# Kernel optimization log

Measured on AMD Instinct MI355X. Metric: run time of the kernel, lower is better.

Reference implementation:

```python
import jax, jax.numpy as jnp
import numpy as np

DIM = 192
RES = 64
NUM_HEADS = 4
H_SP, W_SP = RES, 4  # idx == 0
SCALE = (DIM // NUM_HEADS) ** (-0.5)


def conv2d(x, w, b, pad, groups=1):
    y = jax.lax.conv_general_dilated(
        x, w, window_strides=(1, 1), padding=[(pad, pad), (pad, pad)],
        dimension_numbers=("NCHW", "OIHW", "NCHW"), feature_group_count=groups)
    return y + b[None, :, None, None]


def img2windows(img, H_sp, W_sp):
    B, C, H, W = img.shape
    x = img.reshape(B, C, H // H_sp, H_sp, W // W_sp, W_sp)
    return jnp.transpose(x, (0, 2, 4, 3, 5, 1)).reshape(-1, H_sp * W_sp, C)


def windows2img(w, H_sp, W_sp, H, W):
    Bw = w.shape[0]
    B = Bw // ((H // H_sp) * (W // W_sp))
    x = w.reshape(B, H // H_sp, W // W_sp, H_sp, W_sp, -1)
    return jnp.transpose(x, (0, 5, 1, 3, 2, 4)).reshape(B, -1, H, W)


def im2cswin(x):
    w = img2windows(x, H_SP, W_SP)  # [B', L, C]
    Bw, L, C = w.shape
    return jnp.transpose(w.reshape(Bw, L, NUM_HEADS, C // NUM_HEADS), (0, 2, 1, 3))


def setup_inputs() -> dict:
    key = jax.random.key(0)
    ks = jax.random.split(key, 11)
    s = 0.02
    return {
        "x": jax.random.normal(ks[0], (32, DIM, RES, RES), jnp.float32),
        "w_qk": jax.random.normal(ks[1], (2 * DIM, DIM, 1, 1), jnp.float32) * s,
        "b_qk": jnp.zeros((2 * DIM,), jnp.float32),
        "w_q5": jax.random.normal(ks[2], (DIM, 1, 5, 5), jnp.float32) * s,
        "b_q5": jnp.zeros((DIM,), jnp.float32),
        "w_k5": jax.random.normal(ks[3], (DIM, 1, 5, 5), jnp.float32) * s,
        "b_k5": jnp.zeros((DIM,), jnp.float32),
        "w_v": jax.random.normal(ks[4], (DIM, DIM, 1, 1), jnp.float32) * s,
        "b_v": jnp.zeros((DIM,), jnp.float32),
        "w_cape": jax.random.normal(ks[5], (DIM, 1, 5, 5), jnp.float32) * s,
        "b_cape": jnp.zeros((DIM,), jnp.float32),
    }


def reference(x, w_qk, b_qk, w_q5, b_q5, w_k5, b_k5, w_v, b_v, w_cape, b_cape):
    B, C, H, W = x.shape
    qk = conv2d(x, w_qk, b_qk, pad=0)
    q, k = jnp.split(qk, 2, axis=1)
    v = conv2d(x, w_v, b_v, pad=0)
    cape = conv2d(v, w_cape, b_cape, pad=2, groups=DIM)  # depthwise 5x5
    q = im2cswin(conv2d(q, w_q5, b_q5, pad=2, groups=DIM) + cape)
    k = im2cswin(conv2d(k, w_k5, b_k5, pad=2, groups=DIM) + cape)
    vw = im2cswin(v)
    q = q * SCALE
    attn = jnp.einsum("whqd,whkd->whqk", q, k)  # windows, heads, L, L
    attn = jax.nn.softmax(attn, axis=-1)
    out = jnp.einsum("whqk,whkd->whqd", attn, vw)
    Bw = out.shape[0]
    out = jnp.transpose(out, (0, 2, 1, 3)).reshape(Bw, H_SP * W_SP, C)
    return windows2img(out, H_SP, W_SP, H, W) + cape
```

## Files before the change

### kernel.cpp

```cpp
#include <hip/hip_runtime.h>

typedef short short8 __attribute__((ext_vector_type(8)));
typedef float f32x4 __attribute__((ext_vector_type(4)));

#define BATCH 32
#define DIM 192
#define RES 64
#define HW 4096
#define NH 4
#define DH 48
#define NWIN 16
#define LTOK 256
#define BUFE (BATCH * DIM * HW)
#define SCALE_Q 0.14433756729740643f

__device__ __forceinline__ unsigned short f2bf(float f) {
  unsigned int u = __builtin_bit_cast(unsigned int, f);
  u += 0x7fffu + ((u >> 16) & 1u);
  return (unsigned short)(u >> 16);
}
__device__ __forceinline__ float bf2f(unsigned short h) {
  unsigned int u = ((unsigned int)h) << 16;
  return __builtin_bit_cast(float, u);
}
__device__ __forceinline__ f32x4 mfma16(short8 a, short8 b, f32x4 c) {
  return __builtin_amdgcn_mfma_f32_16x16x32_bf16(a, b, c, 0, 0, 0);
}

__global__ __launch_bounds__(256, 2) void k1_conv1x1(
    const float* __restrict__ x, const float* __restrict__ w_qk,
    const float* __restrict__ b_qk, const float* __restrict__ w_v,
    const float* __restrict__ b_v, unsigned short* __restrict__ q_raw,
    unsigned short* __restrict__ k_raw, unsigned short* __restrict__ v_buf) {
  __shared__ unsigned short Al[96 * 200];
  __shared__ unsigned short Bl[64 * 200];
  const int tid = threadIdx.x;
  const int octile = blockIdx.x;
  const int pixtile = blockIdx.y;
  const int b = blockIdx.z;
  const int oc0 = octile * 96;
  const int pix0 = pixtile * 64;

  {
    const float* wsrc = (oc0 < 384) ? (w_qk + oc0 * DIM) : (w_v + (oc0 - 384) * DIM);
    for (int it = 0; it < 18; ++it) {
      int u = it * 256 + tid;
      int oc = u / 48, ic4 = u % 48;
      float4 f = *(const float4*)(wsrc + oc * DIM + ic4 * 4);
      uint2 pk;
      pk.x = (unsigned int)f2bf(f.x) | ((unsigned int)f2bf(f.y) << 16);
      pk.y = (unsigned int)f2bf(f.z) | ((unsigned int)f2bf(f.w) << 16);
      *(uint2*)&Al[oc * 200 + ic4 * 4] = pk;
    }
  }
  {
    const float* xb = x + (size_t)b * (DIM * HW) + pix0;
    int px = tid & 63;
    int icq = tid >> 6;
    for (int it = 0; it < 6; ++it) {
      int ic8 = icq + it * 4;
      const float* p = xb + (size_t)(ic8 * 8) * HW + px;
      unsigned short h[8];
#pragma unroll
      for (int j = 0; j < 8; ++j) h[j] = f2bf(p[(size_t)j * HW]);
      uint4 pk;
      pk.x = h[0] | ((unsigned int)h[1] << 16);
      pk.y = h[2] | ((unsigned int)h[3] << 16);
      pk.z = h[4] | ((unsigned int)h[5] << 16);
      pk.w = h[6] | ((unsigned int)h[7] << 16);
      *(uint4*)&Bl[px * 200 + ic8 * 8] = pk;
    }
  }
  __syncthreads();

  const int lane = tid & 63, wv = tid >> 6;
  const int quad = lane >> 4, col = lane & 15;
  const int m0 = (wv >> 1) * 48, n0 = (wv & 1) * 32;

  f32x4 acc[3][2];
#pragma unroll
  for (int fm = 0; fm < 3; ++fm)
#pragma unroll
    for (int fn = 0; fn < 2; ++fn) {
      acc[fm][fn][0] = 0.f; acc[fm][fn][1] = 0.f;
      acc[fm][fn][2] = 0.f; acc[fm][fn][3] = 0.f;
    }

#pragma unroll
  for (int ks = 0; ks < 6; ++ks) {
    short8 a[3], bb[2];
#pragma unroll
    for (int fm = 0; fm < 3; ++fm)
      a[fm] = *(const short8*)&Al[(m0 + fm * 16 + col) * 200 + ks * 32 + quad * 8];
#pragma unroll
    for (int fn = 0; fn < 2; ++fn)
      bb[fn] = *(const short8*)&Bl[(n0 + fn * 16 + col) * 200 + ks * 32 + quad * 8];
#pragma unroll
    for (int fm = 0; fm < 3; ++fm)
#pragma unroll
      for (int fn = 0; fn < 2; ++fn) acc[fm][fn] = mfma16(a[fm], bb[fn], acc[fm][fn]);
  }

  unsigned short* dst;
  int ocbase;
  if (oc0 < 192) { dst = q_raw; ocbase = oc0; }
  else if (oc0 < 384) { dst = k_raw; ocbase = oc0 - 192; }
  else { dst = v_buf; ocbase = oc0 - 384; }
#pragma unroll
  for (int fm = 0; fm < 3; ++fm) {
#pragma unroll
    for (int r = 0; r < 4; ++r) {
      int ocoff = m0 + fm * 16 + quad * 4 + r;
      int ocg = oc0 + ocoff;
      float bias = (ocg < 384) ? b_qk[ocg] : b_v[ocg - 384];
      size_t rowoff = ((size_t)b * DIM + (ocbase + ocoff)) * HW;
#pragma unroll
      for (int fn = 0; fn < 2; ++fn) {
        int pix = pix0 + n0 + fn * 16 + col;
        dst[rowoff + pix] = f2bf(acc[fm][fn][r] + bias);
      }
    }
  }
}

__global__ __launch_bounds__(256) void k2_cape(
    const unsigned short* __restrict__ v_buf, const float* __restrict__ w_cape,
    const float* __restrict__ b_cape, float* __restrict__ cape_out) {
  const int c = blockIdx.y, b = blockIdx.z;
  const int h = blockIdx.x * 16 + (threadIdx.x >> 4);
  const int w4 = threadIdx.x & 15;
  const unsigned short* vp = v_buf + ((size_t)b * DIM + c) * HW;
  float wk[25];
#pragma unroll
  for (int i = 0; i < 25; ++i) wk[i] = w_cape[c * 25 + i];
  float acc[4];
  float bz = b_cape[c];
  acc[0] = acc[1] = acc[2] = acc[3] = bz;
#pragma unroll
  for (int dy = 0; dy < 5; ++dy) {
    int hr = h + dy - 2;
    float row[8];
    if (hr >= 0 && hr < RES) {
      const unsigned short* rp = vp + hr * RES + w4 * 4 - 2;
#pragma unroll
      for (int j = 0; j < 4; ++j) {
        int wc = w4 * 4 - 2 + 2 * j;
        unsigned int d = (wc >= 0 && wc < RES) ? *(const unsigned int*)(rp + 2 * j) : 0u;
        row[2 * j] = bf2f((unsigned short)(d & 0xffff));
        row[2 * j + 1] = bf2f((unsigned short)(d >> 16));
      }
    } else {
#pragma unroll
      for (int j = 0; j < 8; ++j) row[j] = 0.f;
    }
#pragma unroll
    for (int wj = 0; wj < 4; ++wj)
#pragma unroll
      for (int dx = 0; dx < 5; ++dx) acc[wj] += row[wj + dx] * wk[dy * 5 + dx];
  }
  float4 o;
  o.x = acc[0]; o.y = acc[1]; o.z = acc[2]; o.w = acc[3];
  *(float4*)&cape_out[((size_t)b * DIM + c) * HW + h * RES + w4 * 4] = o;
}

__global__ __launch_bounds__(256) void k3_dw(
    const unsigned short* __restrict__ src, const float* __restrict__ w5,
    const float* __restrict__ b5, const float* __restrict__ cape,
    unsigned short* __restrict__ dst_w, float scale) {
  __shared__ unsigned short patch[64 * 168];
  __shared__ unsigned short outS[64 * 72];
  const int lid = blockIdx.x;
  const int xx = lid & 7;
  const int ii = lid >> 3;
  const int b = xx * 4 + ii / 192;
  const int rem = ii % 192;
  const int wb = rem / 12;
  const int rr2 = rem % 12;
  const int ct = rr2 >> 2, ht = rr2 & 3;
  const int c0 = ct * 64, h0 = ht * 16;
  const int tid = threadIdx.x;

  for (int it = 0; it < 5; ++it) {
    int u = it * 256 + tid;
    int c = u / 20, rr = u % 20;
    int hr = h0 - 2 + rr;
    uint4 pk;
    pk.x = pk.y = pk.z = pk.w = 0u;
    if (hr >= 0 && hr < RES) {
      const unsigned short* rp =
          src + ((size_t)b * DIM + c0 + c) * HW + hr * RES + wb * 4 - 2;
      unsigned int dw[4];
#pragma unroll
      for (int j = 0; j < 4; ++j) {
        int wc = wb * 4 - 2 + 2 * j;
        dw[j] = (wc >= 0 && wc < RES) ? *(const unsigned int*)(rp + 2 * j) : 0u;
      }
      pk.x = dw[0]; pk.y = dw[1]; pk.z = dw[2]; pk.w = dw[3];
    }
    *(uint4*)&patch[c * 168 + rr * 8] = pk;
  }
  __syncthreads();

  const int c = tid >> 2, hq = tid & 3;
  float wk[25];
#pragma unroll
  for (int i = 0; i < 25; ++i) wk[i] = w5[(c0 + c) * 25 + i];
  float bz = b5[c0 + c];
  float acc[4][4];
#pragma unroll
  for (int j = 0; j < 4; ++j)
#pragma unroll
    for (int wm = 0; wm < 4; ++wm) acc[j][wm] = bz;

#pragma unroll
  for (int rel = 0; rel < 8; ++rel) {
    int p = hq * 4 + rel;
    uint4 pk = *(const uint4*)&patch[c * 168 + p * 8];
    float f8[8];
    f8[0] = bf2f((unsigned short)(pk.x & 0xffff));
    f8[1] = bf2f((unsigned short)(pk.x >> 16));
    f8[2] = bf2f((unsigned short)(pk.y & 0xffff));
    f8[3] = bf2f((unsigned short)(pk.y >> 16));
    f8[4] = bf2f((unsigned short)(pk.z & 0xffff));
    f8[5] = bf2f((unsigned short)(pk.z >> 16));
    f8[6] = bf2f((unsigned short)(pk.w & 0xffff));
    f8[7] = bf2f((unsigned short)(pk.w >> 16));
#pragma unroll
    for (int j = 0; j < 4; ++j) {
      int dy = rel - j;
      if (dy >= 0 && dy <= 4) {
#pragma unroll
        for (int wm = 0; wm < 4; ++wm)
#pragma unroll
          for (int dx = 0; dx < 5; ++dx) acc[j][wm] += f8[wm + dx] * wk[dy * 5 + dx];
      }
    }
  }

  size_t cpbase = ((size_t)b * DIM + c0 + c) * HW + (size_t)wb * 4;
#pragma unroll
  for (int j = 0; j < 4; ++j) {
    int h = h0 + hq * 4 + j;
    float4 cp = *(const float4*)&cape[cpbase + (size_t)h * RES];
    int lb = (hq * 4 + j) * 4;
    outS[(lb + 0) * 72 + c] = f2bf((acc[j][0] + cp.x) * scale);
    outS[(lb + 1) * 72 + c] = f2bf((acc[j][1] + cp.y) * scale);
    outS[(lb + 2) * 72 + c] = f2bf((acc[j][2] + cp.z) * scale);
    outS[(lb + 3) * 72 + c] = f2bf((acc[j][3] + cp.w) * scale);
  }
  __syncthreads();

  const size_t obase = ((size_t)(b * NWIN + wb) * LTOK + (size_t)h0 * 4) * DIM + c0;
  for (int it = 0; it < 2; ++it) {
    int u = it * 256 + tid;
    int ll = u >> 3, part = u & 7;
    *(uint4*)&dst_w[obase + (size_t)ll * DIM + part * 8] =
        *(const uint4*)&outS[ll * 72 + part * 8];
  }
}

#define KSTR 56
#define VSTR 256
#define PSTR 264

__global__ __launch_bounds__(256, 2) void k5_attn(
    const unsigned short* __restrict__ qf_w, const unsigned short* __restrict__ kf_w,
    const unsigned short* __restrict__ v_buf, unsigned short* __restrict__ out_w) {
  __shared__ unsigned short smem[29184];
  unsigned short* Kl = smem;
  unsigned short* Pl = smem;
  unsigned short* Vl = smem + 16896;

  const int lid = blockIdx.x;
  const int xx = lid & 7;
  const int ii = lid >> 3;
  const int b = (xx << 2) | (ii >> 8);
  const int rem = ii & 255;
  const int wb = rem >> 4;
  const int hd = (rem >> 2) & 3;
  const int qt = rem & 3;
  const int wi = b * NWIN + wb;

  const int tid = threadIdx.x, lane = tid & 63, wv = tid >> 6;
  const int quad = lane >> 4, col = lane & 15;
  const int q = qt * 64 + wv * 16 + col;

  const unsigned short* qp = qf_w + ((size_t)wi * LTOK + q) * DIM + hd * DH;
  short8 z8 = {0, 0, 0, 0, 0, 0, 0, 0};
  short8 bq0 = *(const short8*)(qp + quad * 8);
  short8 bq1 = z8;
  if (quad < 2) bq1 = *(const short8*)(qp + 32 + quad * 8);

  {
    const unsigned short* ks = kf_w + (size_t)wi * LTOK * DIM + hd * DH;
    for (int it = 0; it < 6; ++it) {
      int u = it * 256 + tid;
      int kl = u / 6, part = u % 6;
      *(uint4*)&Kl[kl * KSTR + part * 8] = *(const uint4*)(ks + (size_t)kl * DIM + part * 8);
    }
  }
  {
    const unsigned short* vs = v_buf + ((size_t)b * DIM + hd * DH) * HW + wb * 4;
    for (int it = 0; it < 12; ++it) {
      int u = it * 256 + tid;
      int d = u >> 6, h = u & 63;
      int kl8 = h >> 1;
      int off = ((kl8 ^ (d & 7)) * 8) + (h & 1) * 4;
      *(uint2*)&Vl[d * VSTR + off] = *(const uint2*)(vs + (size_t)d * HW + h * RES);
    }
  }
  __syncthreads();

  f32x4 s[16];
#pragma unroll
  for (int i = 0; i < 16; ++i) { s[i][0] = 0.f; s[i][1] = 0.f; s[i][2] = 0.f; s[i][3] = 0.f; }
#pragma unroll
  for (int fm = 0; fm < 16; ++fm) {
    short8 a0 = *(const short8*)&Kl[(fm * 16 + col) * KSTR + quad * 8];
    s[fm] = mfma16(a0, bq0, s[fm]);
  }
#pragma unroll
  for (int fm = 0; fm < 16; ++fm) {
    short8 a1 = z8;
    if (quad < 2) a1 = *(const short8*)&Kl[(fm * 16 + col) * KSTR + 32 + quad * 8];
    s[fm] = mfma16(a1, bq1, s[fm]);
  }

  float mx = s[0][0];
#pragma unroll
  for (int fm = 0; fm < 16; ++fm)
#pragma unroll
    for (int r = 0; r < 4; ++r) mx = fmaxf(mx, s[fm][r]);
  mx = fmaxf(mx, __shfl_xor(mx, 16));
  mx = fmaxf(mx, __shfl_xor(mx, 32));
  float sm = 0.f;
#pragma unroll
  for (int fm = 0; fm < 16; ++fm)
#pragma unroll
    for (int r = 0; r < 4; ++r) {
      float e = __expf(s[fm][r] - mx);
      s[fm][r] = e;
      sm += e;
    }
  sm += __shfl_xor(sm, 16);
  sm += __shfl_xor(sm, 32);
  float inv = 1.f / sm;

  __syncthreads();

  {
    unsigned short* Pw = Pl + (wv * 16 + col) * PSTR;
#pragma unroll
    for (int fm = 0; fm < 16; ++fm) {
      uint2 pk;
      pk.x = (unsigned int)f2bf(s[fm][0] * inv) | ((unsigned int)f2bf(s[fm][1] * inv) << 16);
      pk.y = (unsigned int)f2bf(s[fm][2] * inv) | ((unsigned int)f2bf(s[fm][3] * inv) << 16);
      *(uint2*)&Pw[fm * 16 + quad * 4] = pk;
    }
  }

  f32x4 o[3];
#pragma unroll
  for (int i = 0; i < 3; ++i) { o[i][0] = 0.f; o[i][1] = 0.f; o[i][2] = 0.f; o[i][3] = 0.f; }
#pragma unroll
  for (int ksi = 0; ksi < 8; ++ksi) {
    short8 a = *(const short8*)&Pl[(wv * 16 + col) * PSTR + ksi * 32 + quad * 8];
#pragma unroll
    for (int fn = 0; fn < 3; ++fn) {
      int d = fn * 16 + col;
      short8 bb = *(const short8*)&Vl[d * VSTR + (((ksi * 4 + quad) ^ (d & 7)) * 8)];
      o[fn] = mfma16(a, bb, o[fn]);
    }
  }

  {
    unsigned short* dst = out_w + ((size_t)wi * LTOK + qt * 64 + wv * 16) * DIM + hd * DH;
#pragma unroll
    for (int fn = 0; fn < 3; ++fn)
#pragma unroll
      for (int r = 0; r < 4; ++r)
        dst[(size_t)(quad * 4 + r) * DIM + fn * 16 + col] = f2bf(o[fn][r]);
  }
}

__global__ __launch_bounds__(256) void k6_final(
    const unsigned short* __restrict__ out_w, float* __restrict__ io) {
  __shared__ float tile[16 * 528];
  const int ht = blockIdx.x, ct = blockIdx.y, b = blockIdx.z;
  const int c0 = ct * 16, h0 = ht * 8;
  const int tid = threadIdx.x;
  for (int it = 0; it < 4; ++it) {
    int u = it * 256 + tid;
    int chunk = u & 1, l5 = (u >> 1) & 31, wb = u >> 6;
    const unsigned short* p =
        out_w + ((size_t)(b * NWIN + wb) * LTOK + (size_t)(h0 * 4 + l5)) * DIM + c0 + chunk * 8;
    uint4 pk = *(const uint4*)p;
    int h = l5 >> 2, wm = l5 & 3;
    float* t = &tile[(chunk * 8) * 528 + h * 66 + wb * 4 + wm];
    t[0 * 528] = bf2f((unsigned short)(pk.x & 0xffff));
    t[1 * 528] = bf2f((unsigned short)(pk.x >> 16));
    t[2 * 528] = bf2f((unsigned short)(pk.y & 0xffff));
    t[3 * 528] = bf2f((unsigned short)(pk.y >> 16));
    t[4 * 528] = bf2f((unsigned short)(pk.z & 0xffff));
    t[5 * 528] = bf2f((unsigned short)(pk.z >> 16));
    t[6 * 528] = bf2f((unsigned short)(pk.w & 0xffff));
    t[7 * 528] = bf2f((unsigned short)(pk.w >> 16));
  }
  __syncthreads();
  for (int it = 0; it < 8; ++it) {
    int u = it * 256 + tid;
    int w16 = u & 15, h = (u >> 4) & 7, c = u >> 7;
    size_t g = ((size_t)b * DIM + c0 + c) * HW + (size_t)(h0 + h) * RES + w16 * 4;
    float4 cp = *(const float4*)&io[g];
    float4 ov;
    ov.x = tile[c * 528 + h * 66 + w16 * 4 + 0] + cp.x;
    ov.y = tile[c * 528 + h * 66 + w16 * 4 + 1] + cp.y;
    ov.z = tile[c * 528 + h * 66 + w16 * 4 + 2] + cp.z;
    ov.w = tile[c * 528 + h * 66 + w16 * 4 + 3] + cp.w;
    *(float4*)&io[g] = ov;
  }
}

extern "C" void kernel_launch(void* const* d_in, const int* in_sizes, int n_in,
                              void* d_out, int out_size, void* d_ws, size_t ws_size,
                              hipStream_t stream) {
  (void)in_sizes; (void)n_in; (void)out_size; (void)ws_size;
  const float* x = (const float*)d_in[0];
  const float* w_qk = (const float*)d_in[1];
  const float* b_qk = (const float*)d_in[2];
  const float* w_q5 = (const float*)d_in[3];
  const float* b_q5 = (const float*)d_in[4];
  const float* w_k5 = (const float*)d_in[5];
  const float* b_k5 = (const float*)d_in[6];
  const float* w_v = (const float*)d_in[7];
  const float* b_v = (const float*)d_in[8];
  const float* w_cape = (const float*)d_in[9];
  const float* b_cape = (const float*)d_in[10];
  float* out = (float*)d_out;

  unsigned short* ws = (unsigned short*)d_ws;
  unsigned short* buf0 = ws;
  unsigned short* buf1 = ws + (size_t)BUFE;
  unsigned short* buf2 = ws + (size_t)BUFE * 2;
  unsigned short* buf3 = ws + (size_t)BUFE * 3;

  k1_conv1x1<<<dim3(6, 64, 32), 256, 0, stream>>>(x, w_qk, b_qk, w_v, b_v, buf0, buf1, buf2);
  k2_cape<<<dim3(4, 192, 32), 256, 0, stream>>>(buf2, w_cape, b_cape, out);
  k3_dw<<<dim3(6144), 256, 0, stream>>>(buf0, w_q5, b_q5, out, buf3, SCALE_Q);
  k3_dw<<<dim3(6144), 256, 0, stream>>>(buf1, w_k5, b_k5, out, buf0, 1.0f);
  k5_attn<<<dim3(8192), 256, 0, stream>>>(buf3, buf0, buf2, buf1);
  k6_final<<<dim3(8, 12, 32), 256, 0, stream>>>(buf1, out);
}
```

Before: 780.6 us.

## Pre-convert 1x1 conv weights to bf16 and loop all output-channel tiles per block

Adds a small kernel that converts the qk and v 1x1 weights to bf16 once, written into a scratch buffer. The 1x1 conv kernel now handles all six 96-channel output tiles inside each block. The x tile is converted and staged in shared memory once, so it is no longer re-read and re-converted six times. The next weight tile is prefetched into registers while the current tile is computed, at the cost of higher register use, fewer blocks (2048) and an extra launch.

```diff
diff --git a/kernel.cpp b/kernel.cpp
--- a/kernel.cpp
+++ b/kernel.cpp
@@ -27,32 +27,31 @@
   return __builtin_amdgcn_mfma_f32_16x16x32_bf16(a, b, c, 0, 0, 0);
 }
 
+__global__ __launch_bounds__(256) void k0_wcvt(
+    const float* __restrict__ w_qk, const float* __restrict__ w_v,
+    unsigned short* __restrict__ wbf) {
+  int u = blockIdx.x * 256 + threadIdx.x;
+  int i4 = u * 4;
+  const float* src = (i4 < 2 * DIM * DIM) ? (w_qk + i4) : (w_v + (i4 - 2 * DIM * DIM));
+  float4 f = *(const float4*)src;
+  uint2 pk;
+  pk.x = (unsigned int)f2bf(f.x) | ((unsigned int)f2bf(f.y) << 16);
+  pk.y = (unsigned int)f2bf(f.z) | ((unsigned int)f2bf(f.w) << 16);
+  *(uint2*)&wbf[i4] = pk;
+}
+
 __global__ __launch_bounds__(256, 2) void k1_conv1x1(
-    const float* __restrict__ x, const float* __restrict__ w_qk,
-    const float* __restrict__ b_qk, const float* __restrict__ w_v,
-    const float* __restrict__ b_v, unsigned short* __restrict__ q_raw,
-    unsigned short* __restrict__ k_raw, unsigned short* __restrict__ v_buf) {
+    const float* __restrict__ x, const unsigned short* __restrict__ wbf,
+    const float* __restrict__ b_qk, const float* __restrict__ b_v,
+    unsigned short* __restrict__ q_raw, unsigned short* __restrict__ k_raw,
+    unsigned short* __restrict__ v_buf) {
   __shared__ unsigned short Al[96 * 200];
   __shared__ unsigned short Bl[64 * 200];
   const int tid = threadIdx.x;
-  const int octile = blockIdx.x;
-  const int pixtile = blockIdx.y;
-  const int b = blockIdx.z;
-  const int oc0 = octile * 96;
+  const int pixtile = blockIdx.x;
+  const int b = blockIdx.y;
   const int pix0 = pixtile * 64;
 
-  {
-    const float* wsrc = (oc0 < 384) ? (w_qk + oc0 * DIM) : (w_v + (oc0 - 384) * DIM);
-    for (int it = 0; it < 18; ++it) {
-      int u = it * 256 + tid;
-      int oc = u / 48, ic4 = u % 48;
-      float4 f = *(const float4*)(wsrc + oc * DIM + ic4 * 4);
-      uint2 pk;
-      pk.x = (unsigned int)f2bf(f.x) | ((unsigned int)f2bf(f.y) << 16);
-      pk.y = (unsigned int)f2bf(f.z) | ((unsigned int)f2bf(f.w) << 16);
-      *(uint2*)&Al[oc * 200 + ic4 * 4] = pk;
-    }
-  }
   {
     const float* xb = x + (size_t)b * (DIM * HW) + pix0;
     int px = tid & 63;
@@ -71,55 +70,84 @@
       *(uint4*)&Bl[px * 200 + ic8 * 8] = pk;
     }
   }
-  __syncthreads();
 
   const int lane = tid & 63, wv = tid >> 6;
   const int quad = lane >> 4, col = lane & 15;
   const int m0 = (wv >> 1) * 48, n0 = (wv & 1) * 32;
 
-  f32x4 acc[3][2];
-#pragma unroll
-  for (int fm = 0; fm < 3; ++fm)
-#pragma unroll
-    for (int fn = 0; fn < 2; ++fn) {
-      acc[fm][fn][0] = 0.f; acc[fm][fn][1] = 0.f;
-      acc[fm][fn][2] = 0.f; acc[fm][fn][3] = 0.f;
-    }
-
-#pragma unroll
-  for (int ks = 0; ks < 6; ++ks) {
-    short8 a[3], bb[2];
+  uint4 wreg[9];
+#pragma unroll
+  for (int it = 0; it < 9; ++it) {
+    int u = it * 256 + tid;
+    int row = u / 24, part = u % 24;
+    wreg[it] = *(const uint4*)(wbf + row * 192 + part * 8);
+  }
+
+  for (int t = 0; t < 6; ++t) {
+#pragma unroll
+    for (int it = 0; it < 9; ++it) {
+      int u = it * 256 + tid;
+      int row = u / 24, part = u % 24;
+      *(uint4*)&Al[row * 200 + part * 8] = wreg[it];
+    }
+    __syncthreads();
+
+    if (t < 5) {
+      const unsigned short* wsrc = wbf + (t + 1) * (96 * 192);
+#pragma unroll
+      for (int it = 0; it < 9; ++it) {
+        int u = it * 256 + tid;
+        int row = u / 24, part = u % 24;
+        wreg[it] = *(const uint4*)(wsrc + row * 192 + part * 8);
+      }
+    }
+
+    f32x4 acc[3][2];
 #pragma unroll
     for (int fm = 0; fm < 3; ++fm)
-      a[fm] = *(const short8*)&Al[(m0 + fm * 16 + col) * 200 + ks * 32 + quad * 8];
-#pragma unroll
-    for (int fn = 0; fn < 2; ++fn)
-      bb[fn] = *(const short8*)&Bl[(n0 + fn * 16 + col) * 200 + ks * 32 + quad * 8];
-#pragma unroll
-    for (int fm = 0; fm < 3; ++fm)
-#pragma unroll
-      for (int fn = 0; fn < 2; ++fn) acc[fm][fn] = mfma16(a[fm], bb[fn], acc[fm][fn]);
-  }
-
-  unsigned short* dst;
-  int ocbase;
-  if (oc0 < 192) { dst = q_raw; ocbase = oc0; }
-  else if (oc0 < 384) { dst = k_raw; ocbase = oc0 - 192; }
-  else { dst = v_buf; ocbase = oc0 - 384; }
-#pragma unroll
-  for (int fm = 0; fm < 3; ++fm) {
-#pragma unroll
-    for (int r = 0; r < 4; ++r) {
-      int ocoff = m0 + fm * 16 + quad * 4 + r;
-      int ocg = oc0 + ocoff;
-      float bias = (ocg < 384) ? b_qk[ocg] : b_v[ocg - 384];
-      size_t rowoff = ((size_t)b * DIM + (ocbase + ocoff)) * HW;
 #pragma unroll
       for (int fn = 0; fn < 2; ++fn) {
-        int pix = pix0 + n0 + fn * 16 + col;
-        dst[rowoff + pix] = f2bf(acc[fm][fn][r] + bias);
-      }
-    }
+        acc[fm][fn][0] = 0.f; acc[fm][fn][1] = 0.f;
+        acc[fm][fn][2] = 0.f; acc[fm][fn][3] = 0.f;
+      }
+
+#pragma unroll
+    for (int ks = 0; ks < 6; ++ks) {
+      short8 a[3], bb[2];
+#pragma unroll
+      for (int fm = 0; fm < 3; ++fm)
+        a[fm] = *(const short8*)&Al[(m0 + fm * 16 + col) * 200 + ks * 32 + quad * 8];
+#pragma unroll
+      for (int fn = 0; fn < 2; ++fn)
+        bb[fn] = *(const short8*)&Bl[(n0 + fn * 16 + col) * 200 + ks * 32 + quad * 8];
+#pragma unroll
+      for (int fm = 0; fm < 3; ++fm)
+#pragma unroll
+        for (int fn = 0; fn < 2; ++fn) acc[fm][fn] = mfma16(a[fm], bb[fn], acc[fm][fn]);
+    }
+
+    const int oc0 = t * 96;
+    unsigned short* dst;
+    int ocbase;
+    if (oc0 < 192) { dst = q_raw; ocbase = oc0; }
+    else if (oc0 < 384) { dst = k_raw; ocbase = oc0 - 192; }
+    else { dst = v_buf; ocbase = oc0 - 384; }
+#pragma unroll
+    for (int fm = 0; fm < 3; ++fm) {
+#pragma unroll
+      for (int r = 0; r < 4; ++r) {
+        int ocoff = m0 + fm * 16 + quad * 4 + r;
+        int ocg = oc0 + ocoff;
+        float bias = (ocg < 384) ? b_qk[ocg] : b_v[ocg - 384];
+        size_t rowoff = ((size_t)b * DIM + (ocbase + ocoff)) * HW;
+#pragma unroll
+        for (int fn = 0; fn < 2; ++fn) {
+          int pix = pix0 + n0 + fn * 16 + col;
+          dst[rowoff + pix] = f2bf(acc[fm][fn][r] + bias);
+        }
+      }
+    }
+    __syncthreads();
   }
 }
 
@@ -444,7 +472,8 @@
   unsigned short* buf2 = ws + (size_t)BUFE * 2;
   unsigned short* buf3 = ws + (size_t)BUFE * 3;
 
-  k1_conv1x1<<<dim3(6, 64, 32), 256, 0, stream>>>(x, w_qk, b_qk, w_v, b_v, buf0, buf1, buf2);
+  k0_wcvt<<<dim3(108), 256, 0, stream>>>(w_qk, w_v, buf3);
+  k1_conv1x1<<<dim3(64, 32), 256, 0, stream>>>(x, buf3, b_qk, b_v, buf0, buf1, buf2);
   k2_cape<<<dim3(4, 192, 32), 256, 0, stream>>>(buf2, w_cape, b_cape, out);
   k3_dw<<<dim3(6144), 256, 0, stream>>>(buf0, w_q5, b_q5, out, buf3, SCALE_Q);
   k3_dw<<<dim3(6144), 256, 0, stream>>>(buf1, w_k5, b_k5, out, buf0, 1.0f);
```

Result: slower. 806.3 us (+3.3%).
